# Kernel tuning notes

Hardware: AMD Instinct MI355X
Metric: run time of the kernel (lower is better)

## Reference

```python
import math
import jax, jax.numpy as jnp
import numpy as np

DIM = 2048
NUM_HEADS = 32
NUM_KV_HEADS = 8
HEAD_DIM = DIM // NUM_HEADS
KV_REPEAT = NUM_HEADS // NUM_KV_HEADS
BSZ, SEQ = 2, 2048
THRESHOLD = 0.05


def ternarize_ste(w):
    # scale = mean(|w|), clamped; ternary in {-1,0,1}; STE: fwd value is ternary,
    # grad flows straight through to w.
    scale = jnp.maximum(jnp.abs(w).mean(), 1e-6)
    ternary = jnp.where(w > THRESHOLD * scale, 1.0,
                        jnp.where(w < -THRESHOLD * scale, -1.0, 0.0)).astype(w.dtype)
    return w + jax.lax.stop_gradient(ternary - w)


def setup_inputs() -> dict:
    key = jax.random.key(0)
    kx, kq, kk, kv, ko = jax.random.split(key, 5)
    # kaiming_uniform_(a=sqrt(5)) => U(-b, b) with b = 1/sqrt(in_features)
    bound = 1.0 / math.sqrt(DIM)
    return {
        "x": jax.random.normal(kx, (BSZ, SEQ, DIM), dtype=jnp.float32),
        "wq": jax.random.uniform(kq, (DIM, DIM), jnp.float32, -bound, bound),
        "wk": jax.random.uniform(kk, (HEAD_DIM * NUM_KV_HEADS, DIM), jnp.float32, -bound, bound),
        "wv": jax.random.uniform(kv, (HEAD_DIM * NUM_KV_HEADS, DIM), jnp.float32, -bound, bound),
        "wo": jax.random.uniform(ko, (DIM, DIM), jnp.float32, -bound, bound),
    }


def reference(x, wq, wk, wv, wo):
    bsz, seq, _ = x.shape
    # BitLinear projections with ternarized weights (F.linear: x @ W^T)
    q = x @ ternarize_ste(wq).T                      # [b, s, dim]
    k = x @ ternarize_ste(wk).T                      # [b, s, kvh*hd]
    v = x @ ternarize_ste(wv).T

    q = q.reshape(bsz, seq, NUM_HEADS, HEAD_DIM)     # [b, s, H, d]
    k = k.reshape(bsz, seq, NUM_KV_HEADS, HEAD_DIM)
    v = v.reshape(bsz, seq, NUM_KV_HEADS, HEAD_DIM)
    # repeat_interleave over the kv-head axis to match query heads
    k = jnp.repeat(k, KV_REPEAT, axis=2)             # [b, s, H, d]
    v = jnp.repeat(v, KV_REPEAT, axis=2)

    scale = 1.0 / math.sqrt(HEAD_DIM)
    att = jnp.einsum('bqhd,bkhd->bhqk', q, k) * scale  # [b, H, s, s]
    causal = jnp.tril(jnp.ones((seq, seq), dtype=bool))
    att = jnp.where(causal, att, -jnp.inf)
    probs = jax.nn.softmax(att, axis=-1)
    out = jnp.einsum('bhqk,bkhd->bqhd', probs, v).reshape(bsz, seq, DIM)
    return out @ ternarize_ste(wo).T
```

## Files before the change

### kernel.cpp

```cpp
#include <hip/hip_runtime.h>

typedef _Float16 f16;
typedef f16  f16x8 __attribute__((ext_vector_type(8)));
typedef f16  f16x4 __attribute__((ext_vector_type(4)));
typedef float f32x4 __attribute__((ext_vector_type(4)));

#define DIM_   2048
#define SEQ_   2048
#define BATCH_ 2
#define MROWS_ (BATCH_*SEQ_)
#define HD_    64
#define KVW_   512

__device__ __forceinline__ f32x4 mfma16(f16x8 a, f16x8 b, f32x4 c) {
  return __builtin_amdgcn_mfma_f32_16x16x32_f16(a, b, c, 0, 0, 0);
}

typedef const __attribute__((address_space(1))) void gas_void;
typedef __attribute__((address_space(3))) void las_void;
__device__ __forceinline__ void gload16(const void* g, void* l) {
  __builtin_amdgcn_global_load_lds((gas_void*)g, (las_void*)l, 16, 0, 0);
}

__device__ __forceinline__ unsigned long long pk4(float a, float b, float c, float d) {
  union { _Float16 h[4]; unsigned long long u; } z;
  auto p0 = __builtin_amdgcn_cvt_pkrtz(a, b);
  auto p1 = __builtin_amdgcn_cvt_pkrtz(c, d);
  z.h[0] = p0[0]; z.h[1] = p0[1]; z.h[2] = p1[0]; z.h[3] = p1[1];
  return z.u;
}

__global__ __launch_bounds__(256)
void prep1(const float* __restrict__ x,
           const float* __restrict__ w0, const float* __restrict__ w1,
           const float* __restrict__ w2, const float* __restrict__ w3,
           float* __restrict__ parts, f16* __restrict__ hi, f16* __restrict__ lo) {
  const int id = blockIdx.y;
  if (id < 4) {
    const float* w = id == 0 ? w0 : id == 1 ? w1 : id == 2 ? w2 : w3;
    const int n4 = (id == 1 || id == 2) ? (KVW_ * DIM_ / 4) : (DIM_ * DIM_ / 4);
    float s = 0.f;
    for (int i = blockIdx.x * 256 + threadIdx.x; i < n4; i += gridDim.x * 256) {
      float4 v = *(const float4*)(w + (long)i * 4);
      s += fabsf(v.x) + fabsf(v.y) + fabsf(v.z) + fabsf(v.w);
    }
    #pragma unroll
    for (int off = 32; off > 0; off >>= 1)
      s += __shfl_down(s, off, 64);
    __shared__ float red[4];
    int lane = threadIdx.x & 63, wv = threadIdx.x >> 6;
    if (lane == 0) red[wv] = s;
    __syncthreads();
    if (threadIdx.x == 0)
      parts[id * 192 + blockIdx.x] = (red[0] + red[1]) + (red[2] + red[3]);
  } else {
    const int half = (MROWS_ * DIM_ / 4) / 2;
    const long base = (long)(id - 4) * half;
    for (int i = blockIdx.x * 256 + threadIdx.x; i < half; i += gridDim.x * 256) {
      float4 v = *(const float4*)(x + (base + i) * 4);
      f16x4 h, l;
      h[0] = (f16)v.x; l[0] = (f16)(v.x - (float)h[0]);
      h[1] = (f16)v.y; l[1] = (f16)(v.y - (float)h[1]);
      h[2] = (f16)v.z; l[2] = (f16)(v.z - (float)h[2]);
      h[3] = (f16)v.w; l[3] = (f16)(v.w - (float)h[3]);
      *(f16x4*)(hi + (base + i) * 4) = h;
      *(f16x4*)(lo + (base + i) * 4) = l;
    }
  }
}

__global__ __launch_bounds__(256)
void ternarize4(const float* __restrict__ w0, const float* __restrict__ w1,
                const float* __restrict__ w2, const float* __restrict__ w3,
                unsigned short* __restrict__ t0, unsigned short* __restrict__ t1,
                unsigned short* __restrict__ t2, unsigned short* __restrict__ t3,
                const float* __restrict__ parts) {
  const int id = blockIdx.y;
  const float* w = id == 0 ? w0 : id == 1 ? w1 : id == 2 ? w2 : w3;
  unsigned short* t = id == 0 ? t0 : id == 1 ? t1 : id == 2 ? t2 : t3;
  const int n = (id == 1 || id == 2) ? (KVW_ * DIM_) : (DIM_ * DIM_);

  __shared__ float thr_s;
  if (threadIdx.x < 64) {
    const int lane = threadIdx.x;
    float s = parts[id * 192 + lane] + parts[id * 192 + 64 + lane]
            + parts[id * 192 + 128 + lane];
    #pragma unroll
    for (int off = 32; off > 0; off >>= 1)
      s += __shfl_down(s, off, 64);
    if (lane == 0) thr_s = 0.05f * fmaxf(s / (float)n, 1e-6f);
  }
  __syncthreads();
  const float thr = thr_s;

  const int n4 = n >> 2;
  for (int i = blockIdx.x * 256 + threadIdx.x; i < n4; i += gridDim.x * 256) {
    float4 v = *(const float4*)(w + (long)i * 4);
    ushort4 o;
    o.x = v.x > thr ? 0x3C00 : (v.x < -thr ? 0xBC00 : 0);
    o.y = v.y > thr ? 0x3C00 : (v.y < -thr ? 0xBC00 : 0);
    o.z = v.z > thr ? 0x3C00 : (v.z < -thr ? 0xBC00 : 0);
    o.w = v.w > thr ? 0x3C00 : (v.w < -thr ? 0xBC00 : 0);
    *(ushort4*)(t + (long)i * 4) = o;
  }
}

__global__ __launch_bounds__(128, 2)
void gemm_qkv(const f16* __restrict__ Ah, const f16* __restrict__ Al,
              const f16* __restrict__ Bw,
              f16* __restrict__ O1, f16* __restrict__ O2,
              f16* __restrict__ K1, f16* __restrict__ K2,
              f16* __restrict__ OV) {
  constexpr int BUFSZ = 24576;
  __shared__ __attribute__((aligned(16))) char smem[2 * BUFSZ];

  const int id2 = (blockIdx.x & 7) * 96 + (blockIdx.x >> 3);
  const int bx  = id2 % 24;
  const int by  = id2 / 24;
  const int brow = by * 128;
  const int bcol = bx * 128;

  const int tid  = threadIdx.x;
  const int lane = tid & 63;
  const int wv   = tid >> 6;
  const int wr   = wv * 64;
  const int fr   = lane & 15;
  const int fq   = lane >> 4;

  const bool lo_on = bcol < 2560;

  const int rl  = lane >> 2;
  const int scg = ((lane & 3) ^ ((lane >> 3) & 3)) * 8;
  const f16* gA0 = Ah + (long)(brow + wv * 64 + rl) * DIM_ + scg;
  const f16* gL0 = Al + (long)(brow + wv * 64 + rl) * DIM_ + scg;
  const f16* gB0 = Bw + (long)(bcol + wv * 64 + rl) * DIM_ + scg;
  const int wvb = __builtin_amdgcn_readfirstlane(wv * 2048);

  auto STAGE = [&](int kt, int buf) {
    const int k0 = kt * 32;
    char* base = smem + buf * BUFSZ;
    f16* lA = (f16*)base + wvb;
    f16* lL = (f16*)(base + 8192) + wvb;
    f16* lB = (f16*)(base + 16384) + wvb;
    #pragma unroll
    for (int g = 0; g < 4; ++g) {
      gload16(gA0 + k0 + g * 16 * DIM_, lA + g * 512);
      gload16(gB0 + k0 + g * 16 * DIM_, lB + g * 512);
    }
    if (lo_on) {
      #pragma unroll
      for (int g = 0; g < 4; ++g)
        gload16(gL0 + k0 + g * 16 * DIM_, lL + g * 512);
    }
  };

  const int xga = (fq ^ ((fr >> 1) & 3)) * 8;

  f32x4 acc[4][8] = {};
  const int nk = DIM_ / 32;

  STAGE(0, 0);
  #pragma unroll 1
  for (int kt = 0; kt < nk; ++kt) {
    asm volatile("s_waitcnt vmcnt(0)" ::: "memory");
    __syncthreads();
    if (kt + 1 < nk) STAGE(kt + 1, (kt + 1) & 1);

    const char* base = smem + (kt & 1) * BUFSZ;
    const f16* cAh = (const f16*)base;
    const f16* cAl = (const f16*)(base + 8192);
    const f16* cB  = (const f16*)(base + 16384);

    f16x8 bfr[8];
    #pragma unroll
    for (int ni = 0; ni < 8; ++ni)
      bfr[ni] = *(const f16x8*)(cB + (ni * 16 + fr) * 32 + xga);
    #pragma unroll
    for (int mi = 0; mi < 4; ++mi) {
      const int aoff = (wr + mi * 16 + fr) * 32 + xga;
      f16x8 ah = *(const f16x8*)(cAh + aoff);
      #pragma unroll
      for (int ni = 0; ni < 8; ++ni)
        acc[mi][ni] = mfma16(ah, bfr[ni], acc[mi][ni]);
      if (lo_on) {
        f16x8 al = *(const f16x8*)(cAl + aoff);
        #pragma unroll
        for (int ni = 0; ni < 8; ++ni)
          acc[mi][ni] = mfma16(al, bfr[ni], acc[mi][ni]);
      }
    }
  }

  const int colbase = bcol;
  if (colbase < 2048) {
    #pragma unroll
    for (int mi = 0; mi < 4; ++mi)
      #pragma unroll
      for (int ni = 0; ni < 8; ++ni)
        #pragma unroll
        for (int r = 0; r < 4; ++r) {
          long idx = (long)(brow + wr + mi * 16 + fq * 4 + r) * DIM_
                   + colbase + ni * 16 + fr;
          float v = acc[mi][ni][r];
          f16 hv = (f16)v;
          O1[idx] = hv;
          O2[idx] = (f16)(v - (float)hv);
        }
  } else if (colbase < 2560) {
    #pragma unroll
    for (int mi = 0; mi < 4; ++mi)
      #pragma unroll
      for (int ni = 0; ni < 8; ++ni)
        #pragma unroll
        for (int r = 0; r < 4; ++r) {
          long idx = (long)(brow + wr + mi * 16 + fq * 4 + r) * KVW_
                   + (colbase - 2048) + ni * 16 + fr;
          float v = acc[mi][ni][r];
          f16 hv = (f16)v;
          K1[idx] = hv;
          K2[idx] = (f16)(v - (float)hv);
        }
  } else {
    f16* st = (f16*)smem + wv * 32 * 72;
    const int bb = brow >> 11;
    const int s0 = (brow & (SEQ_ - 1)) + wr;
    #pragma unroll
    for (int nh = 0; nh < 4; ++nh) {
      const int khh = ((colbase - 2560) >> 6) + (nh >> 1);
      const int db  = (nh & 1) * 32;
      #pragma unroll
      for (int nj = 0; nj < 2; ++nj) {
        const int ni = nh * 2 + nj;
        #pragma unroll
        for (int mi = 0; mi < 4; ++mi)
          #pragma unroll
          for (int r = 0; r < 4; ++r)
            st[(nj * 16 + fr) * 72 + mi * 16 + fq * 4 + r] = (f16)acc[mi][ni][r];
      }
      #pragma unroll
      for (int i = 0; i < 4; ++i) {
        int dl = i * 8 + (lane >> 3);
        f16x8 v = *(const f16x8*)(st + dl * 72 + (lane & 7) * 8);
        *(f16x8*)(OV + ((long)(bb * 8 + khh) * 64 + db + dl) * SEQ_
                  + s0 + (lane & 7) * 8) = v;
      }
    }
  }
}

__global__ __launch_bounds__(256)
void gemm_o(const f16* __restrict__ A, const f16* __restrict__ Bw,
            float* __restrict__ C) {
  constexpr int BUFSZ = 16384;
  __shared__ __attribute__((aligned(16))) char smem[2 * BUFSZ];

  const int cpx = gridDim.x >> 3;
  const int id2 = (blockIdx.x & 7) * cpx + (blockIdx.x >> 3);
  const int nbx = DIM_ >> 7;
  const int bx  = id2 % nbx;
  const int by  = id2 / nbx;
  const int brow = by * 128;
  const int bcol = bx * 128;

  const int tid  = threadIdx.x;
  const int lane = tid & 63;
  const int wv   = tid >> 6;
  const int wr   = (wv >> 1) * 64;
  const int wc   = (wv & 1) * 64;
  const int fr   = lane & 15;
  const int fq   = lane >> 4;

  const int srw = wv * 32 + (lane >> 2);
  const int scg = ((lane & 3) ^ ((lane >> 3) & 3)) * 8;
  const f16* gA0 = A + (long)(brow + srw) * DIM_ + scg;
  const f16* gA1 = gA0 + 16 * (long)DIM_;
  const f16* gB0 = Bw + (long)(bcol + srw) * DIM_ + scg;
  const f16* gB1 = gB0 + 16 * (long)DIM_;
  const int wvb = __builtin_amdgcn_readfirstlane(wv * 1024);

  auto STAGE = [&](int kt, int buf) {
    const int k0 = kt * 32;
    char* base = smem + buf * BUFSZ;
    f16* lA = (f16*)base + wvb;
    f16* lB = (f16*)(base + 8192) + wvb;
    gload16(gA0 + k0, lA);
    gload16(gA1 + k0, lA + 512);
    gload16(gB0 + k0, lB);
    gload16(gB1 + k0, lB + 512);
  };

  const int xga = (fq ^ ((fr >> 1) & 3)) * 8;

  f32x4 acc[4][4] = {};
  const int nk = DIM_ >> 5;

  STAGE(0, 0);
  #pragma unroll 1
  for (int kt = 0; kt < nk; ++kt) {
    asm volatile("s_waitcnt vmcnt(0)" ::: "memory");
    __syncthreads();
    if (kt + 1 < nk) STAGE(kt + 1, (kt + 1) & 1);

    const char* base = smem + (kt & 1) * BUFSZ;
    const f16* cA = (const f16*)base;
    const f16* cB = (const f16*)(base + 8192);

    f16x8 bfr[4];
    #pragma unroll
    for (int ni = 0; ni < 4; ++ni)
      bfr[ni] = *(const f16x8*)(cB + (wc + ni * 16 + fr) * 32 + xga);
    #pragma unroll
    for (int mi = 0; mi < 4; ++mi) {
      f16x8 ah = *(const f16x8*)(cA + (wr + mi * 16 + fr) * 32 + xga);
      #pragma unroll
      for (int ni = 0; ni < 4; ++ni)
        acc[mi][ni] = mfma16(ah, bfr[ni], acc[mi][ni]);
    }
  }

  #pragma unroll
  for (int mi = 0; mi < 4; ++mi)
    #pragma unroll
    for (int ni = 0; ni < 4; ++ni)
      #pragma unroll
      for (int r = 0; r < 4; ++r)
        C[(long)(brow + wr + mi * 16 + fq * 4 + r) * DIM_ + (bcol + wc + ni * 16 + fr)]
            = acc[mi][ni][r];
}

__global__ __launch_bounds__(256, 3)
void attn_kernel(const f16* __restrict__ qhi, const f16* __restrict__ qlo,
                 const f16* __restrict__ khi, const f16* __restrict__ klo,
                 const f16* __restrict__ vt,  f16* __restrict__ AO) {
  const int id2   = (blockIdx.x & 7) * 128 + (blockIdx.x >> 3);
  const int local = id2 & 127;
  const int t     = 63 - (local >> 1);
  const int cmb   = (id2 >> 7) * 2 + (local & 1);
  const int kh    = cmb & 7;
  const int b     = cmb >> 3;
  const int tid  = threadIdx.x;
  const int lane = tid & 63;
  const int w    = tid >> 6;
  const int fr   = lane & 15;
  const int fq   = lane >> 4;
  const int h    = kh * 4 + w;
  const int xr   = (fr & 7) << 4;

  __shared__ __attribute__((aligned(16))) char sKh[64 * 128];
  __shared__ __attribute__((aligned(16))) char sKl[64 * 128];
  __shared__ __attribute__((aligned(16))) char sVt[2][64 * 128];
  __shared__ __attribute__((aligned(16))) char sP [4][2][16 * 128];

  const int srow = w * 16 + (lane >> 3);
  const int scol = ((lane & 7) ^ (lane >> 3)) * 8;
  const f16* gK0 = khi + ((long)(b * SEQ_) + srow) * KVW_ + kh * HD_ + scol;
  const f16* gL0 = klo + ((long)(b * SEQ_) + srow) * KVW_ + kh * HD_ + scol;
  const f16* gV0 = vt + ((long)(b * 8 + kh) * HD_ + srow) * SEQ_ + scol;
  const int ldso = __builtin_amdgcn_readfirstlane(w * 2048);

  auto STAGE_K = [&](int kb) {
    const long ko = (long)kb * 64 * KVW_;
    gload16(gK0 + ko,            sKh + ldso);
    gload16(gK0 + ko + 8 * KVW_, sKh + ldso + 1024);
    gload16(gL0 + ko,            sKl + ldso);
    gload16(gL0 + ko + 8 * KVW_, sKl + ldso + 1024);
  };
  auto STAGE_V = [&](int kb, int buf) {
    const long vo = (long)kb * 64;
    gload16(gV0 + vo,            (char*)sVt[buf] + ldso);
    gload16(gV0 + vo + 8 * SEQ_, (char*)sVt[buf] + ldso + 1024);
  };

  char* pw0 = sP[w][0];
  char* pw1 = sP[w][1];
  const float ce = 0.125f * 1.44269504f;

  const int nkv   = (t >> 1) + 1;
  const int qrow0 = t * 32;

  f16x8 qh[2][2], ql[2][2];
  #pragma unroll
  for (int st = 0; st < 2; ++st)
    #pragma unroll
    for (int ks = 0; ks < 2; ++ks) {
      const long qoff = (long)(b * SEQ_ + qrow0 + st * 16 + fr) * DIM_
                      + h * HD_ + ks * 32 + fq * 8;
      qh[st][ks] = *(const f16x8*)(qhi + qoff);
      ql[st][ks] = *(const f16x8*)(qlo + qoff);
    }

  STAGE_K(0);
  STAGE_V(0, 0);

  float m0 = -1e30f, m1 = -1e30f, l0 = 0.f, l1 = 0.f;
  f32x4 o0[4] = {}, o1[4] = {};

  #pragma unroll 1
  for (int kb = 0; kb < nkv; ++kb) {
    asm volatile("s_waitcnt vmcnt(0)" ::: "memory");
    __syncthreads();
    if (kb + 1 < nkv) STAGE_V(kb + 1, (kb + 1) & 1);
    const char* bV = sVt[kb & 1];

    f32x4 s0[4] = {}, s1[4] = {};
    __builtin_amdgcn_s_setprio(1);
    #pragma unroll
    for (int ks = 0; ks < 2; ++ks)
      #pragma unroll
      for (int ni = 0; ni < 4; ++ni) {
        const int rb = (ni * 16 + fr) * 128 + ((ks * 64 + fq * 16) ^ xr);
        f16x8 ah = *(const f16x8*)(sKh + rb);
        f16x8 af = *(const f16x8*)(sKl + rb);
        s0[ni] = mfma16(ah, qh[0][ks], s0[ni]);
        s0[ni] = mfma16(ah, ql[0][ks], s0[ni]);
        s0[ni] = mfma16(af, qh[0][ks], s0[ni]);
        s1[ni] = mfma16(ah, qh[1][ks], s1[ni]);
        s1[ni] = mfma16(ah, ql[1][ks], s1[ni]);
        s1[ni] = mfma16(af, qh[1][ks], s1[ni]);
      }
    __builtin_amdgcn_s_setprio(0);

    __syncthreads();
    if (kb + 1 < nkv) STAGE_K(kb + 1);

    if (kb == nkv - 1) {
      #pragma unroll
      for (int ni = 0; ni < 4; ++ni)
        #pragma unroll
        for (int r = 0; r < 4; ++r) {
          const int kk = ni * 16 + fq * 4 + r;
          if (kk > (t & 1) * 32 + fr)      s0[ni][r] = -1e30f;
          if (kk > (t & 1) * 32 + 16 + fr) s1[ni][r] = -1e30f;
        }
    }

    #pragma unroll
    for (int st = 0; st < 2; ++st) {
      f32x4* s = st ? s1 : s0;
      float& m = st ? m1 : m0;
      float& l = st ? l1 : l0;
      f32x4* o = st ? o1 : o0;
      char* pw = st ? pw1 : pw0;

      float ma = fmaxf(fmaxf(s[0][0], s[0][1]), fmaxf(s[0][2], s[0][3]));
      float mb2 = fmaxf(fmaxf(s[1][0], s[1][1]), fmaxf(s[1][2], s[1][3]));
      float mc = fmaxf(fmaxf(s[2][0], s[2][1]), fmaxf(s[2][2], s[2][3]));
      float md = fmaxf(fmaxf(s[3][0], s[3][1]), fmaxf(s[3][2], s[3][3]));
      float mb = fmaxf(fmaxf(ma, mb2), fmaxf(mc, md));
      mb = fmaxf(mb, __shfl_xor(mb, 16, 64));
      mb = fmaxf(mb, __shfl_xor(mb, 32, 64));

      const float mo = m;
      const bool trig = mb > mo + 64.f;
      const float mn = trig ? mb : mo;
      m = mn;
      const float al = exp2f((mo - mn) * ce);
      const float tt = mn * ce;

      float rs = 0.f;
      #pragma unroll
      for (int ni = 0; ni < 4; ++ni) {
        #pragma unroll
        for (int r = 0; r < 4; ++r) {
          float pv = exp2f(fmaf(s[ni][r], ce, -tt));
          s[ni][r] = pv;
          rs += pv;
        }
        *(unsigned long long*)(pw + ((fr * 128 + ni * 32 + fq * 8) ^ xr)) =
            pk4(s[ni][0], s[ni][1], s[ni][2], s[ni][3]);
      }
      rs += __shfl_xor(rs, 16, 64);
      rs += __shfl_xor(rs, 32, 64);
      l = l * al + rs;

      if (__any(trig)) {
        #pragma unroll
        for (int r = 0; r < 4; ++r) {
          float alr = __shfl(al, ((lane >> 4) << 2) + r, 64);
          o[0][r] *= alr; o[1][r] *= alr; o[2][r] *= alr; o[3][r] *= alr;
        }
      }
    }

    __builtin_amdgcn_s_setprio(1);
    #pragma unroll
    for (int ks = 0; ks < 2; ++ks) {
      const int pb = (fr * 128 + ks * 64 + fq * 16) ^ xr;
      f16x8 pa0 = *(const f16x8*)(pw0 + pb);
      f16x8 pa1 = *(const f16x8*)(pw1 + pb);
      #pragma unroll
      for (int di = 0; di < 4; ++di) {
        f16x8 vf = *(const f16x8*)(bV + (di * 16 + fr) * 128
                                   + ((ks * 64 + fq * 16) ^ xr));
        o0[di] = mfma16(pa0, vf, o0[di]);
        o1[di] = mfma16(pa1, vf, o1[di]);
      }
    }
    __builtin_amdgcn_s_setprio(0);
  }

  #pragma unroll
  for (int st = 0; st < 2; ++st) {
    const f32x4* o = st ? o1 : o0;
    const float l = st ? l1 : l0;
    float linv[4];
    #pragma unroll
    for (int r = 0; r < 4; ++r)
      linv[r] = 1.f / __shfl(l, ((lane >> 4) << 2) + r, 64);
    #pragma unroll
    for (int di = 0; di < 4; ++di)
      #pragma unroll
      for (int r = 0; r < 4; ++r)
        AO[(long)(b * SEQ_ + qrow0 + st * 16 + fq * 4 + r) * DIM_
           + h * HD_ + di * 16 + fr] = (f16)(o[di][r] * linv[r]);
  }
}

extern "C" void kernel_launch(void* const* d_in, const int* in_sizes, int n_in,
                              void* d_out, int out_size, void* d_ws, size_t ws_size,
                              hipStream_t stream) {
  const float* x  = (const float*)d_in[0];
  const float* wq = (const float*)d_in[1];
  const float* wk = (const float*)d_in[2];
  const float* wv = (const float*)d_in[3];
  const float* wo = (const float*)d_in[4];
  char* ws = (char*)d_ws;

  size_t off = 0;
  float* parts = (float*)ws;                off = 4096;
  f16* x_hi  = (f16*)(ws + off);            off += (size_t)MROWS_ * DIM_ * 2;
  f16* x_lo  = (f16*)(ws + off);            off += (size_t)MROWS_ * DIM_ * 2;
  f16* wq_t  = (f16*)(ws + off);            off += (size_t)DIM_ * DIM_ * 2;
  f16* wkv_t = (f16*)(ws + off);            off += (size_t)1024 * DIM_ * 2;
  f16* wo_t  = (f16*)(ws + off);            off += (size_t)DIM_ * DIM_ * 2;
  f16* qhi   = (f16*)(ws + off);            off += (size_t)MROWS_ * DIM_ * 2;
  f16* qlo   = (f16*)(ws + off);            off += (size_t)MROWS_ * DIM_ * 2;
  f16* khi   = (f16*)(ws + off);            off += (size_t)MROWS_ * KVW_ * 2;
  f16* klo   = (f16*)(ws + off);            off += (size_t)MROWS_ * KVW_ * 2;
  f16* vtb   = (f16*)(ws + off);            off += (size_t)BATCH_ * 8 * 64 * SEQ_ * 2;
  f16* ao    = (f16*)(ws + off);            off += (size_t)MROWS_ * DIM_ * 2;

  prep1<<<dim3(192, 6), dim3(256), 0, stream>>>(x, wq, wk, wv, wo,
                                                parts, x_hi, x_lo);
  ternarize4<<<dim3(192, 4), dim3(256), 0, stream>>>(
      wq, wk, wv, wo,
      (unsigned short*)wq_t, (unsigned short*)wkv_t,
      (unsigned short*)(wkv_t + (size_t)KVW_ * DIM_), (unsigned short*)wo_t,
      parts);

  gemm_qkv<<<dim3(768), dim3(128), 0, stream>>>(
      x_hi, x_lo, wq_t, qhi, qlo, khi, klo, vtb);

  attn_kernel<<<dim3(1024), dim3(256), 0, stream>>>(
      qhi, qlo, khi, klo, vtb, ao);

  gemm_o<<<dim3((DIM_ / 128) * (MROWS_ / 128)), dim3(256), 0, stream>>>(
      ao, wo_t, (float*)d_out);
}
```

Before: 277.0 us.

## Reshape QKV GEMM tile to 64x256 with warps split along columns

The QKV projection GEMM tile changes from 128 rows x 128 cols (warps split by rows) to 64 rows x 256 cols (warps split by columns). The two warps now share a single A tile: one warp loads the hi part and the other the lo part, while both load their own 128 columns of B. The block-to-XCD mapping is rearranged so each XCD handles a contiguous band of rows. This is meant to cut redundant A-split loads and improve L2 locality, but the hi/lo mixing boundary (lo_on) now applies at 256-column granularity per block while the output branch is chosen per warp, which needs care.

```diff
diff --git a/kernel.cpp b/kernel.cpp
--- a/kernel.cpp
+++ b/kernel.cpp
@@ -114,16 +114,17 @@
   constexpr int BUFSZ = 24576;
   __shared__ __attribute__((aligned(16))) char smem[2 * BUFSZ];
 
-  const int id2 = (blockIdx.x & 7) * 96 + (blockIdx.x >> 3);
-  const int bx  = id2 % 24;
-  const int by  = id2 / 24;
-  const int brow = by * 128;
-  const int bcol = bx * 128;
+  const int xcd   = blockIdx.x & 7;
+  const int local = blockIdx.x >> 3;
+  const int bx    = local >> 3;
+  const int by    = xcd * 8 + (local & 7);
+  const int brow  = by * 64;
+  const int bcol  = bx * 256;
 
   const int tid  = threadIdx.x;
   const int lane = tid & 63;
   const int wv   = tid >> 6;
-  const int wr   = wv * 64;
+  const int wc   = wv * 128;
   const int fr   = lane & 15;
   const int fq   = lane >> 4;
 
@@ -131,27 +132,29 @@
 
   const int rl  = lane >> 2;
   const int scg = ((lane & 3) ^ ((lane >> 3) & 3)) * 8;
-  const f16* gA0 = Ah + (long)(brow + wv * 64 + rl) * DIM_ + scg;
-  const f16* gL0 = Al + (long)(brow + wv * 64 + rl) * DIM_ + scg;
-  const f16* gB0 = Bw + (long)(bcol + wv * 64 + rl) * DIM_ + scg;
-  const int wvb = __builtin_amdgcn_readfirstlane(wv * 2048);
+  const f16* gA0 = Ah + (long)(brow + rl) * DIM_ + scg;
+  const f16* gL0 = Al + (long)(brow + rl) * DIM_ + scg;
+  const f16* gB0 = Bw + (long)(bcol + wv * 128 + rl) * DIM_ + scg;
+  const int wvbB = __builtin_amdgcn_readfirstlane(wv * 4096);
 
   auto STAGE = [&](int kt, int buf) {
     const int k0 = kt * 32;
     char* base = smem + buf * BUFSZ;
-    f16* lA = (f16*)base + wvb;
-    f16* lL = (f16*)(base + 8192) + wvb;
-    f16* lB = (f16*)(base + 16384) + wvb;
-    #pragma unroll
-    for (int g = 0; g < 4; ++g) {
-      gload16(gA0 + k0 + g * 16 * DIM_, lA + g * 512);
-      gload16(gB0 + k0 + g * 16 * DIM_, lB + g * 512);
-    }
-    if (lo_on) {
+    if (wv == 0) {
+      f16* lA = (f16*)base;
+      #pragma unroll
+      for (int g = 0; g < 4; ++g)
+        gload16(gA0 + k0 + g * 16 * DIM_, lA + g * 512);
+    } else if (lo_on) {
+      f16* lL = (f16*)(base + 4096);
       #pragma unroll
       for (int g = 0; g < 4; ++g)
         gload16(gL0 + k0 + g * 16 * DIM_, lL + g * 512);
     }
+    f16* lB = (f16*)(base + 8192) + wvbB;
+    #pragma unroll
+    for (int g = 0; g < 8; ++g)
+      gload16(gB0 + k0 + g * 16 * DIM_, lB + g * 512);
   };
 
   const int xga = (fq ^ ((fr >> 1) & 3)) * 8;
@@ -168,16 +171,16 @@
 
     const char* base = smem + (kt & 1) * BUFSZ;
     const f16* cAh = (const f16*)base;
-    const f16* cAl = (const f16*)(base + 8192);
-    const f16* cB  = (const f16*)(base + 16384);
+    const f16* cAl = (const f16*)(base + 4096);
+    const f16* cB  = (const f16*)(base + 8192);
 
     f16x8 bfr[8];
     #pragma unroll
     for (int ni = 0; ni < 8; ++ni)
-      bfr[ni] = *(const f16x8*)(cB + (ni * 16 + fr) * 32 + xga);
+      bfr[ni] = *(const f16x8*)(cB + (wc + ni * 16 + fr) * 32 + xga);
     #pragma unroll
     for (int mi = 0; mi < 4; ++mi) {
-      const int aoff = (wr + mi * 16 + fr) * 32 + xga;
+      const int aoff = (mi * 16 + fr) * 32 + xga;
       f16x8 ah = *(const f16x8*)(cAh + aoff);
       #pragma unroll
       for (int ni = 0; ni < 8; ++ni)
@@ -191,7 +194,7 @@
     }
   }
 
-  const int colbase = bcol;
+  const int colbase = bcol + wc;
   if (colbase < 2048) {
     #pragma unroll
     for (int mi = 0; mi < 4; ++mi)
@@ -199,7 +202,7 @@
       for (int ni = 0; ni < 8; ++ni)
         #pragma unroll
         for (int r = 0; r < 4; ++r) {
-          long idx = (long)(brow + wr + mi * 16 + fq * 4 + r) * DIM_
+          long idx = (long)(brow + mi * 16 + fq * 4 + r) * DIM_
                    + colbase + ni * 16 + fr;
           float v = acc[mi][ni][r];
           f16 hv = (f16)v;
@@ -213,7 +216,7 @@
       for (int ni = 0; ni < 8; ++ni)
         #pragma unroll
         for (int r = 0; r < 4; ++r) {
-          long idx = (long)(brow + wr + mi * 16 + fq * 4 + r) * KVW_
+          long idx = (long)(brow + mi * 16 + fq * 4 + r) * KVW_
                    + (colbase - 2048) + ni * 16 + fr;
           float v = acc[mi][ni][r];
           f16 hv = (f16)v;
@@ -223,7 +226,7 @@
   } else {
     f16* st = (f16*)smem + wv * 32 * 72;
     const int bb = brow >> 11;
-    const int s0 = (brow & (SEQ_ - 1)) + wr;
+    const int s0 = brow & (SEQ_ - 1);
     #pragma unroll
     for (int nh = 0; nh < 4; ++nh) {
       const int khh = ((colbase - 2560) >> 6) + (nh >> 1);
```

Result: no change. 272.9 us (-1.5%).
